# Optimization experiments

Measured on AMD Instinct MI355X. Metric: run time of the kernel, lower is better.

The kernel has to match this reference:

```python
import jax, jax.numpy as jnp
import numpy as np

N = 100000   # num_entities
R = 200      # num_relations
D = 128      # hidden_dim
B = 50       # num_bases = min(R, max(25, R//4))
E = 1600000  # num_edges (avg degree 16)
L = 2        # num_layers


def setup_inputs() -> dict:
    key = jax.random.key(0)
    ks = jax.random.split(key, 7)
    scale = 1.0 / np.sqrt(D)
    entity_emb = jax.random.normal(ks[0], (N, D), jnp.float32) * 0.05  # xavier-scale
    comp = jax.random.normal(ks[1], (L, R, B), jnp.float32) * (1.0 / np.sqrt(B))
    basis = jax.random.normal(ks[2], (L, B, D, D), jnp.float32) * scale
    root = jax.random.normal(ks[3], (L, D, D), jnp.float32) * scale
    bias = jnp.zeros((L, D), jnp.float32)
    edge_index = jax.random.randint(ks[4], (2, E), 0, N, dtype=jnp.int64)
    edge_type = jax.random.randint(ks[5], (E,), 0, R, dtype=jnp.int64)
    return dict(entity_emb=entity_emb, comp=comp, basis=basis, root=root,
                bias=bias, edge_index=edge_index, edge_type=edge_type)


def _rgcn_layer(x, comp_l, basis_l, root_l, bias_l, src, dst, etype):
    # Basis-decomposed relation-specific message: msg_e = x[src_e] @ (sum_b comp[etype_e, b] * basis[b])
    c = comp_l[etype]            # [E, B] per-edge basis coefficients
    x_src = x[src]               # [E, D] gathered source features

    def body(acc, inp):
        b_mat, c_b = inp         # b_mat: [D, D], c_b: [E]
        return acc + c_b[:, None] * (x_src @ b_mat), None

    msg0 = jnp.zeros((src.shape[0], x.shape[1]), x.dtype)
    msg, _ = jax.lax.scan(body, msg0, (basis_l, c.T))  # scan over B bases

    # PyG RGCNConv uses mean aggregation PER RELATION: normalize each edge by
    # the number of incoming edges of the same relation at its destination.
    key = dst * R + etype
    cnt = jnp.zeros(N * R, x.dtype).at[key].add(1.0)
    norm = 1.0 / jnp.maximum(cnt[key], 1.0)             # [E]
    agg = jax.ops.segment_sum(msg * norm[:, None], dst, num_segments=N)
    return agg + x @ root_l + bias_l


def reference(entity_emb, comp, basis, root, bias, edge_index, edge_type):
    src, dst = edge_index[0], edge_index[1]
    x = entity_emb
    for l in range(L):
        x = _rgcn_layer(x, comp[l], basis[l], root[l], bias[l], src, dst, edge_type)
        x = jax.nn.relu(x)
        # dropout(p=0.2) is identity in eval mode
    return x
```

## Files before the change

kernel.cpp:

```cpp
#include <hip/hip_runtime.h>
#include <hip/hip_bf16.h>
#include <stdint.h>

#define D_ 128
#define R_ 200
#define B_ 50
#define N_ 100000
#define TE 64
#define RG_ 4
#define MAXC 8

typedef __attribute__((ext_vector_type(8))) short s8b;
typedef __attribute__((ext_vector_type(4))) float f32x4;
typedef __attribute__((ext_vector_type(4))) uint u32x4;


__device__ __forceinline__ ushort f2bf(float f) {
  uint u = __float_as_uint(f);
  return (ushort)((u + 0x7fffu + ((u >> 16) & 1u)) >> 16);
}
__device__ __forceinline__ float bf2f(ushort u) {
  return __uint_as_float(((uint)u) << 16);
}


__global__ __launch_bounds__(256) void k_hist(const int* __restrict__ et, int E, int* __restrict__ hist) {
  __shared__ int h[R_];
  for (int i = threadIdx.x; i < R_; i += 256) h[i] = 0;
  __syncthreads();
  int base = blockIdx.x * 4096;
  for (int j = 0; j < 16; j++) {
    int i = base + j * 256 + threadIdx.x;
    if (i < E) atomicAdd(&h[et[i]], 1);
  }
  __syncthreads();
  for (int i = threadIdx.x; i < R_; i += 256) { int v = h[i]; if (v) atomicAdd(&hist[i], v); }
}

__global__ __launch_bounds__(256) void k_scanRel(const int* __restrict__ hist,
                                                 int* __restrict__ padOff, int* __restrict__ cursor) {
  __shared__ int s[256];
  int tid = threadIdx.x;
  int v = (tid < R_) ? ((hist[tid] + TE - 1) / TE) * TE : 0;
  s[tid] = v;
  __syncthreads();
  for (int off = 1; off < 256; off <<= 1) {
    int t = (tid >= off) ? s[tid - off] : 0;
    __syncthreads();
    s[tid] += t;
    __syncthreads();
  }
  if (tid < R_) { int e = s[tid] - v; padOff[tid] = e; cursor[tid] = e; }
  if (tid == R_ - 1) padOff[R_] = s[tid];
}

__global__ __launch_bounds__(256) void k_scatter(const int* __restrict__ src, const int* __restrict__ dst,
                                                 const int* __restrict__ et, int E,
                                                 int* __restrict__ cursor,
                                                 int2* __restrict__ srcdst, int* __restrict__ deg) {
  __shared__ int h[R_];
  __shared__ int gb[R_];
  for (int i = threadIdx.x; i < R_; i += 256) h[i] = 0;
  __syncthreads();
  int base = blockIdx.x * 4096;
  int lrank[16];
#pragma unroll
  for (int j = 0; j < 16; j++) {
    int i = base + j * 256 + threadIdx.x;
    lrank[j] = (i < E) ? atomicAdd(&h[et[i]], 1) : 0;
  }
  __syncthreads();
  for (int i = threadIdx.x; i < R_; i += 256) { int v = h[i]; gb[i] = v ? atomicAdd(&cursor[i], v) : 0; }
  __syncthreads();
#pragma unroll
  for (int j = 0; j < 16; j++) {
    int i = base + j * 256 + threadIdx.x;
    if (i < E) {
      int r = et[i], d = dst[i];
      int pos = gb[r] + lrank[j];
      int2 sd; sd.x = src[i]; sd.y = d;
      srcdst[pos] = sd;
      atomicAdd(&deg[d], 1);
    }
  }
}

__global__ __launch_bounds__(256) void k_tileRel(const int* __restrict__ padOff, int* __restrict__ tileRel, int uT) {
  int t = blockIdx.x * 256 + threadIdx.x;
  if (t >= uT) return;
  int base = t * TE;
  if (base >= padOff[R_]) { tileRel[t] = 0; return; }
  int lo = 0, hi = R_ - 1;
  while (lo < hi) { int mid = (lo + hi + 1) >> 1; if (padOff[mid] <= base) lo = mid; else hi = mid - 1; }
  tileRel[t] = lo;
}


__global__ __launch_bounds__(256) void k_degPart(const int* __restrict__ deg, int* __restrict__ blkSum) {
  __shared__ int ws_[4];
  int i = blockIdx.x * 256 + threadIdx.x;
  int v = (i < N_) ? deg[i] : 0;
#pragma unroll
  for (int off = 32; off >= 1; off >>= 1) v += __shfl_down(v, off);
  if ((threadIdx.x & 63) == 0) ws_[threadIdx.x >> 6] = v;
  __syncthreads();
  if (threadIdx.x == 0) blkSum[blockIdx.x] = ws_[0] + ws_[1] + ws_[2] + ws_[3];
}

__global__ __launch_bounds__(512) void k_scanBlk(const int* __restrict__ blkSum, int* __restrict__ blkOff, int nblk) {
  __shared__ int s[512];
  int tid = threadIdx.x;
  int v = (tid < nblk) ? blkSum[tid] : 0;
  s[tid] = v;
  __syncthreads();
  for (int off = 1; off < 512; off <<= 1) {
    int t = (tid >= off) ? s[tid - off] : 0;
    __syncthreads();
    s[tid] += t;
    __syncthreads();
  }
  if (tid < nblk) blkOff[tid] = s[tid] - v;
}

__global__ __launch_bounds__(256) void k_writeOff(const int* __restrict__ deg, const int* __restrict__ blkOff,
                                                  int* __restrict__ dstOff, int* __restrict__ cur) {
  __shared__ int s[256];
  int i = blockIdx.x * 256 + threadIdx.x;
  int tid = threadIdx.x;
  int v = (i < N_) ? deg[i] : 0;
  s[tid] = v;
  __syncthreads();
  for (int off = 1; off < 256; off <<= 1) {
    int t = (tid >= off) ? s[tid - off] : 0;
    __syncthreads();
    s[tid] += t;
    __syncthreads();
  }
  int e = blkOff[blockIdx.x] + s[tid] - v;
  if (i < N_) { dstOff[i] = e; cur[i] = e; }
  else if (i == N_) dstOff[N_] = e;
}

__global__ __launch_bounds__(256) void k_scatterDst(const int2* __restrict__ srcdst,
                                                    const int* __restrict__ padOff, int* __restrict__ cur,
                                                    int* __restrict__ posbuf, int plo, int phi) {
  int p = plo + blockIdx.x * 256 + threadIdx.x;
  if (p >= phi || p >= padOff[R_]) return;
  int d = srcdst[p].y;
  if (d < 0) return;
  int j = atomicAdd(&cur[d], 1);
  posbuf[j] = p;
}

__global__ __launch_bounds__(256) void k_copyBound(const int* __restrict__ cur, int* __restrict__ bnd) {
  int d = blockIdx.x * 256 + threadIdx.x;
  if (d < N_) bnd[d] = cur[d];
}


__global__ __launch_bounds__(256) void k_norm(const int* __restrict__ posbuf, const int* __restrict__ dstOff,
                                              const int* __restrict__ tileRel, float* __restrict__ normS) {
  __shared__ int rels[4][128];
  int d = blockIdx.x * 4 + (threadIdx.x >> 6);
  int sub = threadIdx.x >> 6;
  int l = threadIdx.x & 63;
  int s0 = 0, deg = 0;
  if (d < N_) { s0 = dstOff[d]; deg = dstOff[d + 1] - s0; }
  int cap = deg < 128 ? deg : 128;
  int myp[4]; int myr[4];
  for (int j = l, t = 0; j < cap; j += 64, ++t) {
    int p = posbuf[s0 + j];
    int r = tileRel[p >> 6];
    rels[sub][j] = r;
    if (t < 4) { myp[t] = p; myr[t] = r; }
  }
  __syncthreads();
  if (d >= N_) return;
  for (int j = l, t = 0; j < deg; j += 64, ++t) {
    int p, r;
    if (j < 128 && t < 4) { p = myp[t]; r = myr[t]; }
    else { p = posbuf[s0 + j]; r = tileRel[p >> 6]; }
    int cnt = 0;
    for (int k = 0; k < deg; k++) {
      int rk = (k < 128) ? rels[sub][k] : tileRel[posbuf[s0 + k] >> 6];
      cnt += (rk == r) ? 1 : 0;
    }
    normS[p] = 1.0f / (float)(cnt > 0 ? cnt : 1);
  }
}


__global__ __launch_bounds__(256) void k_computeW(const float* __restrict__ comp, const float* __restrict__ basis,
                                                  float* __restrict__ W) {
  __shared__ float c[B_];
  int r = blockIdx.x >> 6;
  int chunk = blockIdx.x & 63;
  if (threadIdx.x < B_) c[threadIdx.x] = comp[r * B_ + threadIdx.x];
  __syncthreads();
  int ij = chunk * 256 + threadIdx.x;
  float acc = 0.f;
#pragma unroll 10
  for (int b = 0; b < B_; b++) acc += c[b] * basis[b * (D_ * D_) + ij];
  W[r * (D_ * D_) + ij] = acc;
}

__global__ __launch_bounds__(256) void k_packW(const float* __restrict__ W, ushort* __restrict__ Wpack) {
  int r = blockIdx.x;
  const float* Wr = W + (size_t)r * (D_ * D_);
  ushort* out = Wpack + (size_t)r * (D_ * D_);
  for (int i = threadIdx.x; i < D_ * D_; i += 256) {
    int j = i & 7, l = (i >> 3) & 63, cg = (i >> 9) & 7, ks = i >> 12;
    int k = ks * 32 + (l >> 4) * 8 + j;
    int n = cg * 16 + (l & 15);
    out[i] = f2bf(Wr[k * D_ + n]);
  }
}

__global__ __launch_bounds__(256) void k_cast(const float* __restrict__ x, ushort* __restrict__ xb, int n8) {
  int i = blockIdx.x * 256 + threadIdx.x;
  if (i >= n8) return;
  const float4* xp = (const float4*)(x + (size_t)i * 8);
  float4 a = xp[0], b = xp[1];
  uint4 pk;
  pk.x = (uint)f2bf(a.x) | ((uint)f2bf(a.y) << 16);
  pk.y = (uint)f2bf(a.z) | ((uint)f2bf(a.w) << 16);
  pk.z = (uint)f2bf(b.x) | ((uint)f2bf(b.y) << 16);
  pk.w = (uint)f2bf(b.z) | ((uint)f2bf(b.w) << 16);
  *(uint4*)(xb + (size_t)i * 8) = pk;
}


__global__ __launch_bounds__(256, 2) void k_root_mfma(
    const ushort* __restrict__ xb, const ushort* __restrict__ rootPack,
    const float* __restrict__ bias, float* __restrict__ y, int nt) {
  __shared__ ushort Wl[D_ * D_];
  __shared__ float stg[4][16 * 132];
  int tstart = blockIdx.x * RG_;
  if (tstart >= nt) return;
  int tend = tstart + RG_; if (tend > nt) tend = nt;
  int w = threadIdx.x >> 6, l = threadIdx.x & 63;
  int q = l >> 4, tx = l & 15;
  int half = l >> 5, l32 = l & 31;
  float* st = stg[w];
  {
    const uint4* wp = (const uint4*)rootPack;
    uint4* wl = (uint4*)Wl;
#pragma unroll
    for (int i = 0; i < 8; ++i) wl[i * 256 + threadIdx.x] = wp[i * 256 + threadIdx.x];
  }
  float bv[8];
#pragma unroll
  for (int cg = 0; cg < 8; ++cg) bv[cg] = bias[cg * 16 + tx];
  s8b a0, a1, a2, a3;
  {
    int gr = tstart * TE + 16 * w + tx; if (gr >= N_) gr = N_ - 1;
    const s8b* xr = (const s8b*)(xb + (size_t)gr * D_);
    a0 = xr[q]; a1 = xr[4 + q]; a2 = xr[8 + q]; a3 = xr[12 + q];
  }
  __syncthreads();
  for (int tile = tstart; tile < tend; ++tile) {
    int base = tile * TE;
    s8b n0, n1, n2, n3;
    bool pre = (tile + 1 < tend);
    if (pre) {
      int gr = base + TE + 16 * w + tx; if (gr >= N_) gr = N_ - 1;
      const s8b* xn = (const s8b*)(xb + (size_t)gr * D_);
      n0 = xn[q]; n1 = xn[4 + q]; n2 = xn[8 + q]; n3 = xn[12 + q];
    }
    f32x4 acc[8];
#pragma unroll
    for (int cg = 0; cg < 8; ++cg) acc[cg] = (f32x4){0.f, 0.f, 0.f, 0.f};
#pragma unroll
    for (int cg = 0; cg < 8; ++cg) {
      s8b b0 = *(const s8b*)&Wl[((0 * 8 + cg) * 64 + l) * 8];
      s8b b1 = *(const s8b*)&Wl[((1 * 8 + cg) * 64 + l) * 8];
      s8b b2 = *(const s8b*)&Wl[((2 * 8 + cg) * 64 + l) * 8];
      s8b b3 = *(const s8b*)&Wl[((3 * 8 + cg) * 64 + l) * 8];
      acc[cg] = __builtin_amdgcn_mfma_f32_16x16x32_bf16(a0, b0, acc[cg], 0, 0, 0);
      acc[cg] = __builtin_amdgcn_mfma_f32_16x16x32_bf16(a1, b1, acc[cg], 0, 0, 0);
      acc[cg] = __builtin_amdgcn_mfma_f32_16x16x32_bf16(a2, b2, acc[cg], 0, 0, 0);
      acc[cg] = __builtin_amdgcn_mfma_f32_16x16x32_bf16(a3, b3, acc[cg], 0, 0, 0);
    }
#pragma unroll
    for (int cg = 0; cg < 8; ++cg)
#pragma unroll
      for (int r = 0; r < 4; ++r)
        st[(4 * q + r) * 132 + cg * 16 + tx] = acc[cg][r] + bv[cg];
    int grBase = base + 16 * w;
#pragma unroll
    for (int k = 0; k < 8; ++k) {
      int row = 2 * k + half;
      int gr = grBase + row;
      f32x4 v = *(const f32x4*)&st[row * 132 + l32 * 4];
      if (gr < N_) *(f32x4*)(y + (size_t)gr * D_ + l32 * 4) = v;
    }
    if (pre) { a0 = n0; a1 = n1; a2 = n2; a3 = n3; }
  }
}


__global__ __launch_bounds__(256, 4) void k_edges_mfma(
    const ushort* __restrict__ xb, const ushort* __restrict__ Wpack,
    const int2* __restrict__ srcdst, const float* __restrict__ normS,
    const int* __restrict__ tileRel, const int* __restrict__ padOff,
    ushort* __restrict__ msg, int tile0, int tile1, int G) {
  __shared__ ushort Wl[D_ * D_];
  __shared__ ushort stg[4][16 * 136];
  int padTot = padOff[R_];
  int w = threadIdx.x >> 6, l = threadIdx.x & 63;
  int q = l >> 4, tx = l & 15;
  int g = l >> 3, m = l & 7;
  ushort* st = stg[w];
  int curRel = -1;
  for (int tb = tile0 + blockIdx.x * G; tb < tile1; tb += gridDim.x * G) {
    if (tb * TE >= padTot) break;
    int tend = tb + G; if (tend > tile1) tend = tile1;
    s8b a0, a1, a2, a3;
    {
      int2 sd = srcdst[tb * TE + 16 * w + tx];
      int sr = sd.x < 0 ? 0 : sd.x;
      const s8b* xr = (const s8b*)(xb + (size_t)sr * D_);
      a0 = xr[q]; a1 = xr[4 + q]; a2 = xr[8 + q]; a3 = xr[12 + q];
    }
    for (int tile = tb; tile < tend; ++tile) {
      int base = tile * TE;
      if (base >= padTot) break;
      int rel = tileRel[tile];
      if (rel != curRel) {
        curRel = rel;
        __syncthreads();
        const uint4* wp = (const uint4*)(Wpack + (size_t)rel * (D_ * D_));
        uint4* wl = (uint4*)Wl;
#pragma unroll
        for (int i = 0; i < 8; ++i) wl[i * 256 + threadIdx.x] = wp[i * 256 + threadIdx.x];
        __syncthreads();
      }
      float nv[4];
#pragma unroll
      for (int r = 0; r < 4; ++r) nv[r] = normS[base + 16 * w + 4 * q + r];
      s8b n0, n1, n2, n3;
      int nb = base + TE;
      bool pre = (tile + 1 < tend) && (nb < padTot);
      if (pre) {
        int2 sd = srcdst[nb + 16 * w + tx];
        int sr = sd.x < 0 ? 0 : sd.x;
        const s8b* xn = (const s8b*)(xb + (size_t)sr * D_);
        n0 = xn[q]; n1 = xn[4 + q]; n2 = xn[8 + q]; n3 = xn[12 + q];
      }
      f32x4 acc[8];
#pragma unroll
      for (int cg = 0; cg < 8; ++cg) acc[cg] = (f32x4){0.f, 0.f, 0.f, 0.f};
#pragma unroll
      for (int cg = 0; cg < 8; ++cg) {
        s8b b0 = *(const s8b*)&Wl[((0 * 8 + cg) * 64 + l) * 8];
        s8b b1 = *(const s8b*)&Wl[((1 * 8 + cg) * 64 + l) * 8];
        s8b b2 = *(const s8b*)&Wl[((2 * 8 + cg) * 64 + l) * 8];
        s8b b3 = *(const s8b*)&Wl[((3 * 8 + cg) * 64 + l) * 8];
        acc[cg] = __builtin_amdgcn_mfma_f32_16x16x32_bf16(a0, b0, acc[cg], 0, 0, 0);
        acc[cg] = __builtin_amdgcn_mfma_f32_16x16x32_bf16(a1, b1, acc[cg], 0, 0, 0);
        acc[cg] = __builtin_amdgcn_mfma_f32_16x16x32_bf16(a2, b2, acc[cg], 0, 0, 0);
        acc[cg] = __builtin_amdgcn_mfma_f32_16x16x32_bf16(a3, b3, acc[cg], 0, 0, 0);
      }
#pragma unroll
      for (int cg = 0; cg < 8; ++cg)
#pragma unroll
        for (int r = 0; r < 4; ++r)
          st[(4 * q + r) * 136 + cg * 16 + tx] = f2bf(acc[cg][r] * nv[r]);
      ushort* mbase = msg + (size_t)(base - tile0 * TE + 16 * w) * D_;
#pragma unroll
      for (int jj = 0; jj < 2; ++jj)
#pragma unroll
        for (int hh = 0; hh < 2; ++hh) {
          int row = 8 * jj + g;
          u32x4 v = *(const u32x4*)&st[row * 136 + hh * 64 + m * 8];
          *(u32x4*)(mbase + (size_t)row * D_ + hh * 64 + m * 8) = v;
        }
      if (pre) { a0 = n0; a1 = n1; a2 = n2; a3 = n3; }
    }
  }
}


__global__ __launch_bounds__(256) void k_agg2(const ushort* __restrict__ msg, const int* __restrict__ posbuf,
                                              const int* __restrict__ jlo, const int* __restrict__ jhi,
                                              float* __restrict__ y, ushort* __restrict__ xbOut,
                                              int plo, int mode) {
  int d = blockIdx.x * 4 + (threadIdx.x >> 6);
  if (d >= N_) return;
  int l = threadIdx.x & 63, sub = l >> 4, tx = l & 15;
  int s0 = jlo[d], s1 = jhi[d];
  float acc[8];
#pragma unroll
  for (int i = 0; i < 8; ++i) acc[i] = 0.f;
  for (int j = s0 + sub; j < s1; j += 4) {
    int p = posbuf[j];
    u32x4 mv = *(const u32x4*)(msg + (((size_t)(p - plo)) << 7) + (tx << 3));
    acc[0] += bf2f((ushort)mv[0]); acc[1] += bf2f((ushort)(mv[0] >> 16));
    acc[2] += bf2f((ushort)mv[1]); acc[3] += bf2f((ushort)(mv[1] >> 16));
    acc[4] += bf2f((ushort)mv[2]); acc[5] += bf2f((ushort)(mv[2] >> 16));
    acc[6] += bf2f((ushort)mv[3]); acc[7] += bf2f((ushort)(mv[3] >> 16));
  }
#pragma unroll
  for (int i = 0; i < 8; ++i) {
    acc[i] += __shfl_xor(acc[i], 16);
    acc[i] += __shfl_xor(acc[i], 32);
  }
  if (sub == 0) {
    float* yp = y + (((size_t)d) << 7) + (tx << 3);
    float4 y0 = *(float4*)yp, y1 = *(float4*)(yp + 4);
    y0.x += acc[0]; y0.y += acc[1]; y0.z += acc[2]; y0.w += acc[3];
    y1.x += acc[4]; y1.y += acc[5]; y1.z += acc[6]; y1.w += acc[7];
    if (mode == 0) {
      *(float4*)yp = y0; *(float4*)(yp + 4) = y1;
    } else {
      y0.x = fmaxf(y0.x, 0.f); y0.y = fmaxf(y0.y, 0.f); y0.z = fmaxf(y0.z, 0.f); y0.w = fmaxf(y0.w, 0.f);
      y1.x = fmaxf(y1.x, 0.f); y1.y = fmaxf(y1.y, 0.f); y1.z = fmaxf(y1.z, 0.f); y1.w = fmaxf(y1.w, 0.f);
      if (mode == 1) {
        *(float4*)yp = y0; *(float4*)(yp + 4) = y1;
      } else {
        uint4 pk;
        pk.x = (uint)f2bf(y0.x) | ((uint)f2bf(y0.y) << 16);
        pk.y = (uint)f2bf(y0.z) | ((uint)f2bf(y0.w) << 16);
        pk.z = (uint)f2bf(y1.x) | ((uint)f2bf(y1.y) << 16);
        pk.w = (uint)f2bf(y1.z) | ((uint)f2bf(y1.w) << 16);
        *(uint4*)(xbOut + (((size_t)d) << 7) + (tx << 3)) = pk;
      }
    }
  }
}


extern "C" void kernel_launch(void* const* d_in, const int* in_sizes, int n_in,
                              void* d_out, int out_size, void* d_ws, size_t ws_size,
                              hipStream_t stream) {
  const float* entity = (const float*)d_in[0];
  const float* comp   = (const float*)d_in[1];
  const float* basis  = (const float*)d_in[2];
  const float* root   = (const float*)d_in[3];
  const float* bias   = (const float*)d_in[4];
  const int*   eidx   = (const int*)d_in[5];
  const int*   etype  = (const int*)d_in[6];
  const int E = in_sizes[6];
  const int* src = eidx;
  const int* dst = eidx + E;

  char* ws = (char*)d_ws;
  const size_t Epad = (size_t)E + (size_t)R_ * TE;
  const int uTiles = (E + TE - 1) / TE + R_;
  const int NBLK = (N_ + 1 + 255) / 256;
  auto al = [](size_t x) { return (x + 255) & ~(size_t)255; };

  size_t o_Wpack  = 0;
  size_t o_srcdst = al(o_Wpack + (size_t)(R_ + 1) * D_ * D_ * 2);
  size_t o_normS  = al(o_srcdst + Epad * 8);
  size_t o_posbuf = al(o_normS + Epad * 4);
  size_t o_degDst = al(o_posbuf + (size_t)E * 4);
  size_t o_dstOff = al(o_degDst + (size_t)N_ * 4);
  size_t o_cursD  = al(o_dstOff + (size_t)(N_ + 8) * 4);
  size_t o_bounds = al(o_cursD + (size_t)N_ * 4);
  size_t o_tileRel= al(o_bounds + (size_t)MAXC * N_ * 4);
  size_t o_small  = al(o_tileRel + (size_t)uTiles * 4);
  size_t o_y1     = al(o_small + 8192);
  size_t o_xb     = al(o_y1 + (size_t)N_ * D_ * 4);
  size_t o_msg    = al(o_xb + (size_t)N_ * D_ * 2);

  size_t o_Wf     = o_msg;

  ushort* Wpack  = (ushort*)(ws + o_Wpack);
  int2*   srcdst = (int2*)(ws + o_srcdst);
  float*  normS  = (float*)(ws + o_normS);
  int*    posbuf = (int*)(ws + o_posbuf);
  int*    degDst = (int*)(ws + o_degDst);
  int*    dstOff = (int*)(ws + o_dstOff);
  int*    cursD  = (int*)(ws + o_cursD);
  int*    bounds = (int*)(ws + o_bounds);
  int*    tileRel= (int*)(ws + o_tileRel);
  int*    hist   = (int*)(ws + o_small);
  int*    padOff = hist + 256;
  int*    cursor = hist + 512;
  int*    blkSum = hist + 768;
  int*    blkOff = hist + 1280;
  float*  y1     = (float*)(ws + o_y1);
  ushort* xb     = (ushort*)(ws + o_xb);
  float*  Wf     = (float*)(ws + o_Wf);
  ushort* msg    = (ushort*)(ws + o_msg);
  ushort* rootPack = Wpack + (size_t)R_ * D_ * D_;

  (void)hipMemsetAsync(ws + o_srcdst, 0xFF, Epad * 8, stream);
  (void)hipMemsetAsync(ws + o_degDst, 0, (size_t)N_ * 4, stream);
  (void)hipMemsetAsync(ws + o_small, 0, 8192, stream);

  int gH = (E + 4095) / 4096;
  k_hist<<<gH, 256, 0, stream>>>(etype, E, hist);
  k_scanRel<<<1, 256, 0, stream>>>(hist, padOff, cursor);
  k_scatter<<<gH, 256, 0, stream>>>(src, dst, etype, E, cursor, srcdst, degDst);
  k_tileRel<<<(uTiles + 255) / 256, 256, 0, stream>>>(padOff, tileRel, uTiles);
  k_degPart<<<NBLK, 256, 0, stream>>>(degDst, blkSum);
  k_scanBlk<<<1, 512, 0, stream>>>(blkSum, blkOff, NBLK);
  k_writeOff<<<NBLK, 256, 0, stream>>>(degDst, blkOff, dstOff, cursD);

  size_t cap = (ws_size > o_msg + 16384) ? (ws_size - o_msg) : (size_t)16384;
  size_t tileBytes = (size_t)TE * D_ * 2;
  long long maxT = (long long)(cap / tileBytes);
  if (maxT < 1) maxT = 1;
  int nch = (int)((uTiles + maxT - 1) / maxT);
  if (nch < 1) nch = 1;
  size_t totalMsg = (size_t)uTiles * tileBytes;
  int nchT = (int)((totalMsg + ((size_t)136 << 20) - 1) / ((size_t)136 << 20));
  if (nch < nchT) nch = nchT;
  if (nch > MAXC) nch = MAXC;
  int chunkTiles = (uTiles + nch - 1) / nch;
  nch = (uTiles + chunkTiles - 1) / chunkTiles;

  for (int c = 0; c < nch; c++) {
    int plo = c * chunkTiles * TE;
    int phi = (c + 1) * chunkTiles * TE; if (phi > uTiles * TE) phi = uTiles * TE;
    int gS = (phi - plo + 255) / 256;
    if (gS > 0)
      k_scatterDst<<<gS, 256, 0, stream>>>(srcdst, padOff, cursD, posbuf, plo, phi);
    k_copyBound<<<(N_ + 255) / 256, 256, 0, stream>>>(cursD, bounds + (size_t)c * N_);
  }

  k_norm<<<(N_ + 3) / 4, 256, 0, stream>>>(posbuf, dstOff, tileRel, normS);

  int ntR = (N_ + TE - 1) / TE;
  int gAgg = (N_ + 3) / 4;
  k_cast<<<(N_ * D_ / 8 + 255) / 256, 256, 0, stream>>>(entity, xb, N_ * D_ / 8);
  for (int l = 0; l < 2; l++) {
    float* yout = l ? (float*)d_out : y1;
    k_computeW<<<R_ * 64, 256, 0, stream>>>(comp + l * R_ * B_, basis + (size_t)l * B_ * D_ * D_, Wf);
    k_packW<<<R_, 256, 0, stream>>>(Wf, Wpack);
    k_packW<<<1, 256, 0, stream>>>(root + (size_t)l * D_ * D_, rootPack);
    k_root_mfma<<<(ntR + RG_ - 1) / RG_, 256, 0, stream>>>(xb, rootPack, bias + l * D_, yout, ntR);
    for (int c = 0; c < nch; c++) {
      int t0 = c * chunkTiles;
      int t1 = t0 + chunkTiles; if (t1 > uTiles) t1 = uTiles;
      int tiles = t1 - t0;
      int G = (tiles + 1023) / 1024; if (G < 4) G = 4;
      int gB = (tiles + G - 1) / G;
      k_edges_mfma<<<gB, 256, 0, stream>>>(xb, Wpack, srcdst, normS, tileRel, padOff, msg, t0, t1, G);
      const int* jlo = (c == 0) ? dstOff : bounds + (size_t)(c - 1) * N_;
      const int* jhi = bounds + (size_t)c * N_;
      int mode = (c == nch - 1) ? (l ? 1 : 2) : 0;
      k_agg2<<<gAgg, 256, 0, stream>>>(msg, posbuf, jlo, jhi, yout, xb, t0 * TE, mode);
    }
  }
}
```

Before: 1.040 ms.

## Build dst-sorted position buffer via per-chunk counts and ranks instead of atomic cursors

The per-destination counting moves into the relation scatter kernel. It now counts edges per chunk and destination and records each edge's rank within its chunk/destination bucket. Chunk base offsets per destination are derived from these counts, and posbuf is filled in a single atomic-free pass. This replaces the per-chunk scatterDst/copyBound launch loop, which did atomic cursor increments. The cost is an extra rank array, an MAXC*N count array and its memset, plus two small extra kernels.

```diff
diff --git a/kernel.cpp b/kernel.cpp
--- a/kernel.cpp
+++ b/kernel.cpp
@@ -57,7 +57,8 @@
 __global__ __launch_bounds__(256) void k_scatter(const int* __restrict__ src, const int* __restrict__ dst,
                                                  const int* __restrict__ et, int E,
                                                  int* __restrict__ cursor,
-                                                 int2* __restrict__ srcdst, int* __restrict__ deg) {
+                                                 int2* __restrict__ srcdst, int* __restrict__ rankS,
+                                                 int* __restrict__ cntCD, int chunkP) {
   __shared__ int h[R_];
   __shared__ int gb[R_];
   for (int i = threadIdx.x; i < R_; i += 256) h[i] = 0;
@@ -80,7 +81,8 @@
       int pos = gb[r] + lrank[j];
       int2 sd; sd.x = src[i]; sd.y = d;
       srcdst[pos] = sd;
-      atomicAdd(&deg[d], 1);
+      int c = pos / chunkP;
+      rankS[pos] = atomicAdd(&cntCD[c * N_ + d], 1);
     }
   }
 }
@@ -96,6 +98,14 @@
 }
 
 
+__global__ __launch_bounds__(256) void k_deg(const int* __restrict__ cntCD, int* __restrict__ deg, int nch) {
+  int d = blockIdx.x * 256 + threadIdx.x;
+  if (d >= N_) return;
+  int s = 0;
+  for (int c = 0; c < nch; ++c) s += cntCD[c * N_ + d];
+  deg[d] = s;
+}
+
 __global__ __launch_bounds__(256) void k_degPart(const int* __restrict__ deg, int* __restrict__ blkSum) {
   __shared__ int ws_[4];
   int i = blockIdx.x * 256 + threadIdx.x;
@@ -123,7 +133,7 @@
 }
 
 __global__ __launch_bounds__(256) void k_writeOff(const int* __restrict__ deg, const int* __restrict__ blkOff,
-                                                  int* __restrict__ dstOff, int* __restrict__ cur) {
+                                                  int* __restrict__ dstOff) {
   __shared__ int s[256];
   int i = blockIdx.x * 256 + threadIdx.x;
   int tid = threadIdx.x;
@@ -137,24 +147,27 @@
     __syncthreads();
   }
   int e = blkOff[blockIdx.x] + s[tid] - v;
-  if (i < N_) { dstOff[i] = e; cur[i] = e; }
+  if (i < N_) dstOff[i] = e;
   else if (i == N_) dstOff[N_] = e;
 }
 
-__global__ __launch_bounds__(256) void k_scatterDst(const int2* __restrict__ srcdst,
-                                                    const int* __restrict__ padOff, int* __restrict__ cur,
-                                                    int* __restrict__ posbuf, int plo, int phi) {
-  int p = plo + blockIdx.x * 256 + threadIdx.x;
-  if (p >= phi || p >= padOff[R_]) return;
+__global__ __launch_bounds__(256) void k_base(const int* __restrict__ cntCD, const int* __restrict__ dstOff,
+                                              int* __restrict__ base, int nch) {
+  int d = blockIdx.x * 256 + threadIdx.x;
+  if (d >= N_) return;
+  int b = dstOff[d];
+  for (int c = 0; c < nch; ++c) { base[c * N_ + d] = b; b += cntCD[c * N_ + d]; }
+}
+
+__global__ __launch_bounds__(256) void k_buildPos(const int2* __restrict__ srcdst, const int* __restrict__ rankS,
+                                                  const int* __restrict__ base, int* __restrict__ posbuf,
+                                                  int chunkP, int pTot) {
+  int p = blockIdx.x * 256 + threadIdx.x;
+  if (p >= pTot) return;
   int d = srcdst[p].y;
   if (d < 0) return;
-  int j = atomicAdd(&cur[d], 1);
-  posbuf[j] = p;
-}
-
-__global__ __launch_bounds__(256) void k_copyBound(const int* __restrict__ cur, int* __restrict__ bnd) {
-  int d = blockIdx.x * 256 + threadIdx.x;
-  if (d < N_) bnd[d] = cur[d];
+  int c = p / chunkP;
+  posbuf[base[c * N_ + d] + rankS[p]] = p;
 }
 
 
@@ -454,11 +467,12 @@
   size_t o_srcdst = al(o_Wpack + (size_t)(R_ + 1) * D_ * D_ * 2);
   size_t o_normS  = al(o_srcdst + Epad * 8);
   size_t o_posbuf = al(o_normS + Epad * 4);
-  size_t o_degDst = al(o_posbuf + (size_t)E * 4);
+  size_t o_rankS  = al(o_posbuf + (size_t)E * 4);
+  size_t o_degDst = al(o_rankS + Epad * 4);
   size_t o_dstOff = al(o_degDst + (size_t)N_ * 4);
-  size_t o_cursD  = al(o_dstOff + (size_t)(N_ + 8) * 4);
-  size_t o_bounds = al(o_cursD + (size_t)N_ * 4);
-  size_t o_tileRel= al(o_bounds + (size_t)MAXC * N_ * 4);
+  size_t o_base   = al(o_dstOff + (size_t)(N_ + 8) * 4);
+  size_t o_cntCD  = al(o_base + (size_t)MAXC * N_ * 4);
+  size_t o_tileRel= al(o_cntCD + (size_t)MAXC * N_ * 4);
   size_t o_small  = al(o_tileRel + (size_t)uTiles * 4);
   size_t o_y1     = al(o_small + 8192);
   size_t o_xb     = al(o_y1 + (size_t)N_ * D_ * 4);
@@ -470,10 +484,11 @@
   int2*   srcdst = (int2*)(ws + o_srcdst);
   float*  normS  = (float*)(ws + o_normS);
   int*    posbuf = (int*)(ws + o_posbuf);
+  int*    rankS  = (int*)(ws + o_rankS);
   int*    degDst = (int*)(ws + o_degDst);
   int*    dstOff = (int*)(ws + o_dstOff);
-  int*    cursD  = (int*)(ws + o_cursD);
-  int*    bounds = (int*)(ws + o_bounds);
+  int*    base_  = (int*)(ws + o_base);
+  int*    cntCD  = (int*)(ws + o_cntCD);
   int*    tileRel= (int*)(ws + o_tileRel);
   int*    hist   = (int*)(ws + o_small);
   int*    padOff = hist + 256;
@@ -485,19 +500,6 @@
   float*  Wf     = (float*)(ws + o_Wf);
   ushort* msg    = (ushort*)(ws + o_msg);
   ushort* rootPack = Wpack + (size_t)R_ * D_ * D_;
-
-  (void)hipMemsetAsync(ws + o_srcdst, 0xFF, Epad * 8, stream);
-  (void)hipMemsetAsync(ws + o_degDst, 0, (size_t)N_ * 4, stream);
-  (void)hipMemsetAsync(ws + o_small, 0, 8192, stream);
-
-  int gH = (E + 4095) / 4096;
-  k_hist<<<gH, 256, 0, stream>>>(etype, E, hist);
-  k_scanRel<<<1, 256, 0, stream>>>(hist, padOff, cursor);
-  k_scatter<<<gH, 256, 0, stream>>>(src, dst, etype, E, cursor, srcdst, degDst);
-  k_tileRel<<<(uTiles + 255) / 256, 256, 0, stream>>>(padOff, tileRel, uTiles);
-  k_degPart<<<NBLK, 256, 0, stream>>>(degDst, blkSum);
-  k_scanBlk<<<1, 512, 0, stream>>>(blkSum, blkOff, NBLK);
-  k_writeOff<<<NBLK, 256, 0, stream>>>(degDst, blkOff, dstOff, cursD);
 
   size_t cap = (ws_size > o_msg + 16384) ? (ws_size - o_msg) : (size_t)16384;
   size_t tileBytes = (size_t)TE * D_ * 2;
@@ -511,16 +513,23 @@
   if (nch > MAXC) nch = MAXC;
   int chunkTiles = (uTiles + nch - 1) / nch;
   nch = (uTiles + chunkTiles - 1) / chunkTiles;
-
-  for (int c = 0; c < nch; c++) {
-    int plo = c * chunkTiles * TE;
-    int phi = (c + 1) * chunkTiles * TE; if (phi > uTiles * TE) phi = uTiles * TE;
-    int gS = (phi - plo + 255) / 256;
-    if (gS > 0)
-      k_scatterDst<<<gS, 256, 0, stream>>>(srcdst, padOff, cursD, posbuf, plo, phi);
-    k_copyBound<<<(N_ + 255) / 256, 256, 0, stream>>>(cursD, bounds + (size_t)c * N_);
-  }
-
+  int chunkP = chunkTiles * TE;
+
+  (void)hipMemsetAsync(ws + o_srcdst, 0xFF, Epad * 8, stream);
+  (void)hipMemsetAsync(ws + o_cntCD, 0, (size_t)MAXC * N_ * 4, stream);
+  (void)hipMemsetAsync(ws + o_small, 0, 8192, stream);
+
+  int gH = (E + 4095) / 4096;
+  k_hist<<<gH, 256, 0, stream>>>(etype, E, hist);
+  k_scanRel<<<1, 256, 0, stream>>>(hist, padOff, cursor);
+  k_scatter<<<gH, 256, 0, stream>>>(src, dst, etype, E, cursor, srcdst, rankS, cntCD, chunkP);
+  k_tileRel<<<(uTiles + 255) / 256, 256, 0, stream>>>(padOff, tileRel, uTiles);
+  k_deg<<<(N_ + 255) / 256, 256, 0, stream>>>(cntCD, degDst, nch);
+  k_degPart<<<NBLK, 256, 0, stream>>>(degDst, blkSum);
+  k_scanBlk<<<1, 512, 0, stream>>>(blkSum, blkOff, NBLK);
+  k_writeOff<<<NBLK, 256, 0, stream>>>(degDst, blkOff, dstOff);
+  k_base<<<(N_ + 255) / 256, 256, 0, stream>>>(cntCD, dstOff, base_, nch);
+  k_buildPos<<<(uTiles * TE + 255) / 256, 256, 0, stream>>>(srcdst, rankS, base_, posbuf, chunkP, uTiles * TE);
   k_norm<<<(N_ + 3) / 4, 256, 0, stream>>>(posbuf, dstOff, tileRel, normS);
 
   int ntR = (N_ + TE - 1) / TE;
@@ -539,8 +548,8 @@
       int G = (tiles + 1023) / 1024; if (G < 4) G = 4;
       int gB = (tiles + G - 1) / G;
       k_edges_mfma<<<gB, 256, 0, stream>>>(xb, Wpack, srcdst, normS, tileRel, padOff, msg, t0, t1, G);
-      const int* jlo = (c == 0) ? dstOff : bounds + (size_t)(c - 1) * N_;
-      const int* jhi = bounds + (size_t)c * N_;
+      const int* jlo = base_ + (size_t)c * N_;
+      const int* jhi = (c == nch - 1) ? (dstOff + 1) : (base_ + (size_t)(c + 1) * N_);
       int mode = (c == nch - 1) ? (l ? 1 : 2) : 0;
       k_agg2<<<gAgg, 256, 0, stream>>>(msg, posbuf, jlo, jhi, yout, xb, t0 * TE, mode);
     }
```

Measured after the change: 973.7 us. -6.4%, faster.

## Partition edges by destination chunk so each chunk aggregates only its own nodes

Applied to the files above, without the earlier changes.

Edges are now bucketed by (destination chunk, relation) instead of by relation alone. Each message chunk therefore covers a disjoint range of destination nodes, and the aggregation kernel only visits that range instead of all nodes on every chunk, so the per-chunk bound arrays and read-modify-write passes go away. The dst-sorted position buffer is now built in one pass from per-edge ranks, replacing the chunked atomic scatter and bound copies. In exchange the edge records grow to int4, there are up to MAXC*R buckets and so more padding tiles, and a second bf16 activation buffer is added so the layer input is not overwritten while later chunks still read it.

```diff
diff --git a/kernel.cpp b/kernel.cpp
--- a/kernel.cpp
+++ b/kernel.cpp
@@ -9,6 +9,7 @@
 #define TE 64
 #define RG_ 4
 #define MAXC 8
+#define NBMAX (MAXC * R_)
 
 typedef __attribute__((ext_vector_type(8))) short s8b;
 typedef __attribute__((ext_vector_type(4))) float f32x4;
@@ -24,24 +25,126 @@
 }
 
 
-__global__ __launch_bounds__(256) void k_hist(const int* __restrict__ et, int E, int* __restrict__ hist) {
-  __shared__ int h[R_];
-  for (int i = threadIdx.x; i < R_; i += 256) h[i] = 0;
+__global__ __launch_bounds__(256) void k_hist(const int* __restrict__ dst, const int* __restrict__ et,
+                                              int E, int* __restrict__ hist, int DCH, int NB) {
+  __shared__ int h[NBMAX];
+  for (int i = threadIdx.x; i < NB; i += 256) h[i] = 0;
   __syncthreads();
   int base = blockIdx.x * 4096;
   for (int j = 0; j < 16; j++) {
     int i = base + j * 256 + threadIdx.x;
-    if (i < E) atomicAdd(&h[et[i]], 1);
-  }
-  __syncthreads();
-  for (int i = threadIdx.x; i < R_; i += 256) { int v = h[i]; if (v) atomicAdd(&hist[i], v); }
-}
-
-__global__ __launch_bounds__(256) void k_scanRel(const int* __restrict__ hist,
-                                                 int* __restrict__ padOff, int* __restrict__ cursor) {
+    if (i < E) {
+      int key = (dst[i] / DCH) * R_ + et[i];
+      atomicAdd(&h[key], 1);
+    }
+  }
+  __syncthreads();
+  for (int i = threadIdx.x; i < NB; i += 256) { int v = h[i]; if (v) atomicAdd(&hist[i], v); }
+}
+
+__global__ __launch_bounds__(1024) void k_scanRel(const int* __restrict__ hist,
+                                                  int* __restrict__ padOff, int* __restrict__ cursor, int NB) {
+  __shared__ int s[1024];
+  int tid = threadIdx.x;
+  int i0 = 2 * tid, i1 = 2 * tid + 1;
+  int v0 = (i0 < NB) ? ((hist[i0] + TE - 1) / TE) * TE : 0;
+  int v1 = (i1 < NB) ? ((hist[i1] + TE - 1) / TE) * TE : 0;
+  int v = v0 + v1;
+  s[tid] = v;
+  __syncthreads();
+  for (int off = 1; off < 1024; off <<= 1) {
+    int t = (tid >= off) ? s[tid - off] : 0;
+    __syncthreads();
+    s[tid] += t;
+    __syncthreads();
+  }
+  int e = s[tid] - v;
+  if (i0 < NB) { padOff[i0] = e; cursor[i0] = e; }
+  if (i1 < NB) { padOff[i1] = e + v0; cursor[i1] = e + v0; }
+  if (tid == 1023) padOff[NB] = s[1023];
+}
+
+__global__ __launch_bounds__(256) void k_scatter(const int* __restrict__ src, const int* __restrict__ dst,
+                                                 const int* __restrict__ et, int E,
+                                                 int* __restrict__ cursor,
+                                                 int4* __restrict__ sd4, int* __restrict__ cnt,
+                                                 int DCH, int NB) {
+  __shared__ int h[NBMAX];
+  __shared__ int gb[NBMAX];
+  for (int i = threadIdx.x; i < NB; i += 256) h[i] = 0;
+  __syncthreads();
+  int base = blockIdx.x * 4096;
+  int lrank[16];
+#pragma unroll
+  for (int j = 0; j < 16; j++) {
+    int i = base + j * 256 + threadIdx.x;
+    lrank[j] = 0;
+    if (i < E) {
+      int key = (dst[i] / DCH) * R_ + et[i];
+      lrank[j] = atomicAdd(&h[key], 1);
+    }
+  }
+  __syncthreads();
+  for (int i = threadIdx.x; i < NB; i += 256) { int v = h[i]; gb[i] = v ? atomicAdd(&cursor[i], v) : 0; }
+  __syncthreads();
+#pragma unroll
+  for (int j = 0; j < 16; j++) {
+    int i = base + j * 256 + threadIdx.x;
+    if (i < E) {
+      int d = dst[i];
+      int key = (d / DCH) * R_ + et[i];
+      int pos = gb[key] + lrank[j];
+      int rank = atomicAdd(&cnt[d], 1);
+      int4 sd; sd.x = src[i]; sd.y = d; sd.z = rank; sd.w = 0;
+      sd4[pos] = sd;
+    }
+  }
+}
+
+__global__ __launch_bounds__(256) void k_tileRel(const int* __restrict__ padOff, int* __restrict__ tileRel,
+                                                 int uT, int NB) {
+  int t = blockIdx.x * 256 + threadIdx.x;
+  if (t >= uT) return;
+  int base = t * TE;
+  if (base >= padOff[NB]) { tileRel[t] = 0; return; }
+  int lo = 0, hi = NB - 1;
+  while (lo < hi) { int mid = (lo + hi + 1) >> 1; if (padOff[mid] <= base) lo = mid; else hi = mid - 1; }
+  tileRel[t] = lo % R_;
+}
+
+
+__global__ __launch_bounds__(256) void k_degPart(const int* __restrict__ deg, int* __restrict__ blkSum) {
+  __shared__ int ws_[4];
+  int i = blockIdx.x * 256 + threadIdx.x;
+  int v = (i < N_) ? deg[i] : 0;
+#pragma unroll
+  for (int off = 32; off >= 1; off >>= 1) v += __shfl_down(v, off);
+  if ((threadIdx.x & 63) == 0) ws_[threadIdx.x >> 6] = v;
+  __syncthreads();
+  if (threadIdx.x == 0) blkSum[blockIdx.x] = ws_[0] + ws_[1] + ws_[2] + ws_[3];
+}
+
+__global__ __launch_bounds__(512) void k_scanBlk(const int* __restrict__ blkSum, int* __restrict__ blkOff, int nblk) {
+  __shared__ int s[512];
+  int tid = threadIdx.x;
+  int v = (tid < nblk) ? blkSum[tid] : 0;
+  s[tid] = v;
+  __syncthreads();
+  for (int off = 1; off < 512; off <<= 1) {
+    int t = (tid >= off) ? s[tid - off] : 0;
+    __syncthreads();
+    s[tid] += t;
+    __syncthreads();
+  }
+  if (tid < nblk) blkOff[tid] = s[tid] - v;
+}
+
+__global__ __launch_bounds__(256) void k_writeOff(const int* __restrict__ deg, const int* __restrict__ blkOff,
+                                                  int* __restrict__ dstOff) {
   __shared__ int s[256];
+  int i = blockIdx.x * 256 + threadIdx.x;
   int tid = threadIdx.x;
-  int v = (tid < R_) ? ((hist[tid] + TE - 1) / TE) * TE : 0;
+  int v = (i < N_) ? deg[i] : 0;
   s[tid] = v;
   __syncthreads();
   for (int off = 1; off < 256; off <<= 1) {
@@ -50,111 +153,18 @@
     s[tid] += t;
     __syncthreads();
   }
-  if (tid < R_) { int e = s[tid] - v; padOff[tid] = e; cursor[tid] = e; }
-  if (tid == R_ - 1) padOff[R_] = s[tid];
-}
-
-__global__ __launch_bounds__(256) void k_scatter(const int* __restrict__ src, const int* __restrict__ dst,
-                                                 const int* __restrict__ et, int E,
-                                                 int* __restrict__ cursor,
-                                                 int2* __restrict__ srcdst, int* __restrict__ deg) {
-  __shared__ int h[R_];
-  __shared__ int gb[R_];
-  for (int i = threadIdx.x; i < R_; i += 256) h[i] = 0;
-  __syncthreads();
-  int base = blockIdx.x * 4096;
-  int lrank[16];
-#pragma unroll
-  for (int j = 0; j < 16; j++) {
-    int i = base + j * 256 + threadIdx.x;
-    lrank[j] = (i < E) ? atomicAdd(&h[et[i]], 1) : 0;
-  }
-  __syncthreads();
-  for (int i = threadIdx.x; i < R_; i += 256) { int v = h[i]; gb[i] = v ? atomicAdd(&cursor[i], v) : 0; }
-  __syncthreads();
-#pragma unroll
-  for (int j = 0; j < 16; j++) {
-    int i = base + j * 256 + threadIdx.x;
-    if (i < E) {
-      int r = et[i], d = dst[i];
-      int pos = gb[r] + lrank[j];
-      int2 sd; sd.x = src[i]; sd.y = d;
-      srcdst[pos] = sd;
-      atomicAdd(&deg[d], 1);
-    }
-  }
-}
-
-__global__ __launch_bounds__(256) void k_tileRel(const int* __restrict__ padOff, int* __restrict__ tileRel, int uT) {
-  int t = blockIdx.x * 256 + threadIdx.x;
-  if (t >= uT) return;
-  int base = t * TE;
-  if (base >= padOff[R_]) { tileRel[t] = 0; return; }
-  int lo = 0, hi = R_ - 1;
-  while (lo < hi) { int mid = (lo + hi + 1) >> 1; if (padOff[mid] <= base) lo = mid; else hi = mid - 1; }
-  tileRel[t] = lo;
-}
-
-
-__global__ __launch_bounds__(256) void k_degPart(const int* __restrict__ deg, int* __restrict__ blkSum) {
-  __shared__ int ws_[4];
-  int i = blockIdx.x * 256 + threadIdx.x;
-  int v = (i < N_) ? deg[i] : 0;
-#pragma unroll
-  for (int off = 32; off >= 1; off >>= 1) v += __shfl_down(v, off);
-  if ((threadIdx.x & 63) == 0) ws_[threadIdx.x >> 6] = v;
-  __syncthreads();
-  if (threadIdx.x == 0) blkSum[blockIdx.x] = ws_[0] + ws_[1] + ws_[2] + ws_[3];
-}
-
-__global__ __launch_bounds__(512) void k_scanBlk(const int* __restrict__ blkSum, int* __restrict__ blkOff, int nblk) {
-  __shared__ int s[512];
-  int tid = threadIdx.x;
-  int v = (tid < nblk) ? blkSum[tid] : 0;
-  s[tid] = v;
-  __syncthreads();
-  for (int off = 1; off < 512; off <<= 1) {
-    int t = (tid >= off) ? s[tid - off] : 0;
-    __syncthreads();
-    s[tid] += t;
-    __syncthreads();
-  }
-  if (tid < nblk) blkOff[tid] = s[tid] - v;
-}
-
-__global__ __launch_bounds__(256) void k_writeOff(const int* __restrict__ deg, const int* __restrict__ blkOff,
-                                                  int* __restrict__ dstOff, int* __restrict__ cur) {
-  __shared__ int s[256];
-  int i = blockIdx.x * 256 + threadIdx.x;
-  int tid = threadIdx.x;
-  int v = (i < N_) ? deg[i] : 0;
-  s[tid] = v;
-  __syncthreads();
-  for (int off = 1; off < 256; off <<= 1) {
-    int t = (tid >= off) ? s[tid - off] : 0;
-    __syncthreads();
-    s[tid] += t;
-    __syncthreads();
-  }
   int e = blkOff[blockIdx.x] + s[tid] - v;
-  if (i < N_) { dstOff[i] = e; cur[i] = e; }
+  if (i < N_) dstOff[i] = e;
   else if (i == N_) dstOff[N_] = e;
 }
 
-__global__ __launch_bounds__(256) void k_scatterDst(const int2* __restrict__ srcdst,
-                                                    const int* __restrict__ padOff, int* __restrict__ cur,
-                                                    int* __restrict__ posbuf, int plo, int phi) {
-  int p = plo + blockIdx.x * 256 + threadIdx.x;
-  if (p >= phi || p >= padOff[R_]) return;
-  int d = srcdst[p].y;
-  if (d < 0) return;
-  int j = atomicAdd(&cur[d], 1);
-  posbuf[j] = p;
-}
-
-__global__ __launch_bounds__(256) void k_copyBound(const int* __restrict__ cur, int* __restrict__ bnd) {
-  int d = blockIdx.x * 256 + threadIdx.x;
-  if (d < N_) bnd[d] = cur[d];
+__global__ __launch_bounds__(256) void k_buildPos(const int4* __restrict__ sd4, const int* __restrict__ dstOff,
+                                                  int* __restrict__ posbuf, int pTot) {
+  int p = blockIdx.x * 256 + threadIdx.x;
+  if (p >= pTot) return;
+  int4 sd = sd4[p];
+  if (sd.y < 0) return;
+  posbuf[dstOff[sd.y] + sd.z] = p;
 }
 
 
@@ -301,30 +311,32 @@
 
 __global__ __launch_bounds__(256, 4) void k_edges_mfma(
     const ushort* __restrict__ xb, const ushort* __restrict__ Wpack,
-    const int2* __restrict__ srcdst, const float* __restrict__ normS,
+    const int4* __restrict__ sd4, const float* __restrict__ normS,
     const int* __restrict__ tileRel, const int* __restrict__ padOff,
-    ushort* __restrict__ msg, int tile0, int tile1, int G) {
+    ushort* __restrict__ msg, int c) {
   __shared__ ushort Wl[D_ * D_];
   __shared__ ushort stg[4][16 * 136];
-  int padTot = padOff[R_];
+  int b0 = padOff[c * R_], b1 = padOff[(c + 1) * R_];
+  int tile0 = b0 >> 6, tile1 = b1 >> 6;
+  int tiles = tile1 - tile0;
+  if (tiles <= 0) return;
+  int G = (tiles + (int)gridDim.x - 1) / (int)gridDim.x;
   int w = threadIdx.x >> 6, l = threadIdx.x & 63;
   int q = l >> 4, tx = l & 15;
   int g = l >> 3, m = l & 7;
   ushort* st = stg[w];
   int curRel = -1;
-  for (int tb = tile0 + blockIdx.x * G; tb < tile1; tb += gridDim.x * G) {
-    if (tb * TE >= padTot) break;
+  for (int tb = tile0 + blockIdx.x * G; tb < tile1; tb += (int)gridDim.x * G) {
     int tend = tb + G; if (tend > tile1) tend = tile1;
     s8b a0, a1, a2, a3;
     {
-      int2 sd = srcdst[tb * TE + 16 * w + tx];
+      int4 sd = sd4[tb * TE + 16 * w + tx];
       int sr = sd.x < 0 ? 0 : sd.x;
       const s8b* xr = (const s8b*)(xb + (size_t)sr * D_);
       a0 = xr[q]; a1 = xr[4 + q]; a2 = xr[8 + q]; a3 = xr[12 + q];
     }
     for (int tile = tb; tile < tend; ++tile) {
       int base = tile * TE;
-      if (base >= padTot) break;
       int rel = tileRel[tile];
       if (rel != curRel) {
         curRel = rel;
@@ -339,10 +351,9 @@
 #pragma unroll
       for (int r = 0; r < 4; ++r) nv[r] = normS[base + 16 * w + 4 * q + r];
       s8b n0, n1, n2, n3;
-      int nb = base + TE;
-      bool pre = (tile + 1 < tend) && (nb < padTot);
+      bool pre = (tile + 1 < tend);
       if (pre) {
-        int2 sd = srcdst[nb + 16 * w + tx];
+        int4 sd = sd4[base + TE + 16 * w + tx];
         int sr = sd.x < 0 ? 0 : sd.x;
         const s8b* xn = (const s8b*)(xb + (size_t)sr * D_);
         n0 = xn[q]; n1 = xn[4 + q]; n2 = xn[8 + q]; n3 = xn[12 + q];
@@ -352,21 +363,21 @@
       for (int cg = 0; cg < 8; ++cg) acc[cg] = (f32x4){0.f, 0.f, 0.f, 0.f};
 #pragma unroll
       for (int cg = 0; cg < 8; ++cg) {
-        s8b b0 = *(const s8b*)&Wl[((0 * 8 + cg) * 64 + l) * 8];
-        s8b b1 = *(const s8b*)&Wl[((1 * 8 + cg) * 64 + l) * 8];
-        s8b b2 = *(const s8b*)&Wl[((2 * 8 + cg) * 64 + l) * 8];
-        s8b b3 = *(const s8b*)&Wl[((3 * 8 + cg) * 64 + l) * 8];
-        acc[cg] = __builtin_amdgcn_mfma_f32_16x16x32_bf16(a0, b0, acc[cg], 0, 0, 0);
-        acc[cg] = __builtin_amdgcn_mfma_f32_16x16x32_bf16(a1, b1, acc[cg], 0, 0, 0);
-        acc[cg] = __builtin_amdgcn_mfma_f32_16x16x32_bf16(a2, b2, acc[cg], 0, 0, 0);
-        acc[cg] = __builtin_amdgcn_mfma_f32_16x16x32_bf16(a3, b3, acc[cg], 0, 0, 0);
+        s8b b0v = *(const s8b*)&Wl[((0 * 8 + cg) * 64 + l) * 8];
+        s8b b1v = *(const s8b*)&Wl[((1 * 8 + cg) * 64 + l) * 8];
+        s8b b2v = *(const s8b*)&Wl[((2 * 8 + cg) * 64 + l) * 8];
+        s8b b3v = *(const s8b*)&Wl[((3 * 8 + cg) * 64 + l) * 8];
+        acc[cg] = __builtin_amdgcn_mfma_f32_16x16x32_bf16(a0, b0v, acc[cg], 0, 0, 0);
+        acc[cg] = __builtin_amdgcn_mfma_f32_16x16x32_bf16(a1, b1v, acc[cg], 0, 0, 0);
+        acc[cg] = __builtin_amdgcn_mfma_f32_16x16x32_bf16(a2, b2v, acc[cg], 0, 0, 0);
+        acc[cg] = __builtin_amdgcn_mfma_f32_16x16x32_bf16(a3, b3v, acc[cg], 0, 0, 0);
       }
 #pragma unroll
       for (int cg = 0; cg < 8; ++cg)
 #pragma unroll
         for (int r = 0; r < 4; ++r)
           st[(4 * q + r) * 136 + cg * 16 + tx] = f2bf(acc[cg][r] * nv[r]);
-      ushort* mbase = msg + (size_t)(base - tile0 * TE + 16 * w) * D_;
+      ushort* mbase = msg + (size_t)(base - b0 + 16 * w) * D_;
 #pragma unroll
       for (int jj = 0; jj < 2; ++jj)
 #pragma unroll
@@ -382,13 +393,14 @@
 
 
 __global__ __launch_bounds__(256) void k_agg2(const ushort* __restrict__ msg, const int* __restrict__ posbuf,
-                                              const int* __restrict__ jlo, const int* __restrict__ jhi,
+                                              const int* __restrict__ dstOff, const int* __restrict__ padOff,
                                               float* __restrict__ y, ushort* __restrict__ xbOut,
-                                              int plo, int mode) {
-  int d = blockIdx.x * 4 + (threadIdx.x >> 6);
-  if (d >= N_) return;
+                                              int c, int dlo, int dhi, int mode) {
+  int d = dlo + blockIdx.x * 4 + (threadIdx.x >> 6);
+  if (d >= dhi) return;
+  int plo = padOff[c * R_];
   int l = threadIdx.x & 63, sub = l >> 4, tx = l & 15;
-  int s0 = jlo[d], s1 = jhi[d];
+  int s0 = dstOff[d], s1 = dstOff[d + 1];
   float acc[8];
 #pragma unroll
   for (int i = 0; i < 8; ++i) acc[i] = 0.f;
@@ -408,23 +420,19 @@
   if (sub == 0) {
     float* yp = y + (((size_t)d) << 7) + (tx << 3);
     float4 y0 = *(float4*)yp, y1 = *(float4*)(yp + 4);
-    y0.x += acc[0]; y0.y += acc[1]; y0.z += acc[2]; y0.w += acc[3];
-    y1.x += acc[4]; y1.y += acc[5]; y1.z += acc[6]; y1.w += acc[7];
-    if (mode == 0) {
+    y0.x = fmaxf(y0.x + acc[0], 0.f); y0.y = fmaxf(y0.y + acc[1], 0.f);
+    y0.z = fmaxf(y0.z + acc[2], 0.f); y0.w = fmaxf(y0.w + acc[3], 0.f);
+    y1.x = fmaxf(y1.x + acc[4], 0.f); y1.y = fmaxf(y1.y + acc[5], 0.f);
+    y1.z = fmaxf(y1.z + acc[6], 0.f); y1.w = fmaxf(y1.w + acc[7], 0.f);
+    if (mode == 1) {
       *(float4*)yp = y0; *(float4*)(yp + 4) = y1;
     } else {
-      y0.x = fmaxf(y0.x, 0.f); y0.y = fmaxf(y0.y, 0.f); y0.z = fmaxf(y0.z, 0.f); y0.w = fmaxf(y0.w, 0.f);
-      y1.x = fmaxf(y1.x, 0.f); y1.y = fmaxf(y1.y, 0.f); y1.z = fmaxf(y1.z, 0.f); y1.w = fmaxf(y1.w, 0.f);
-      if (mode == 1) {
-        *(float4*)yp = y0; *(float4*)(yp + 4) = y1;
-      } else {
-        uint4 pk;
-        pk.x = (uint)f2bf(y0.x) | ((uint)f2bf(y0.y) << 16);
-        pk.y = (uint)f2bf(y0.z) | ((uint)f2bf(y0.w) << 16);
-        pk.z = (uint)f2bf(y1.x) | ((uint)f2bf(y1.y) << 16);
-        pk.w = (uint)f2bf(y1.z) | ((uint)f2bf(y1.w) << 16);
-        *(uint4*)(xbOut + (((size_t)d) << 7) + (tx << 3)) = pk;
-      }
+      uint4 pk;
+      pk.x = (uint)f2bf(y0.x) | ((uint)f2bf(y0.y) << 16);
+      pk.y = (uint)f2bf(y0.z) | ((uint)f2bf(y0.w) << 16);
+      pk.z = (uint)f2bf(y1.x) | ((uint)f2bf(y1.y) << 16);
+      pk.w = (uint)f2bf(y1.z) | ((uint)f2bf(y1.w) << 16);
+      *(uint4*)(xbOut + (((size_t)d) << 7) + (tx << 3)) = pk;
     }
   }
 }
@@ -445,104 +453,87 @@
   const int* dst = eidx + E;
 
   char* ws = (char*)d_ws;
-  const size_t Epad = (size_t)E + (size_t)R_ * TE;
-  const int uTiles = (E + TE - 1) / TE + R_;
+  const int baseTiles = (E + TE - 1) / TE;
+  const int uTmax = baseTiles + NBMAX;
   const int NBLK = (N_ + 1 + 255) / 256;
   auto al = [](size_t x) { return (x + 255) & ~(size_t)255; };
 
   size_t o_Wpack  = 0;
-  size_t o_srcdst = al(o_Wpack + (size_t)(R_ + 1) * D_ * D_ * 2);
-  size_t o_normS  = al(o_srcdst + Epad * 8);
-  size_t o_posbuf = al(o_normS + Epad * 4);
-  size_t o_degDst = al(o_posbuf + (size_t)E * 4);
-  size_t o_dstOff = al(o_degDst + (size_t)N_ * 4);
-  size_t o_cursD  = al(o_dstOff + (size_t)(N_ + 8) * 4);
-  size_t o_bounds = al(o_cursD + (size_t)N_ * 4);
-  size_t o_tileRel= al(o_bounds + (size_t)MAXC * N_ * 4);
-  size_t o_small  = al(o_tileRel + (size_t)uTiles * 4);
-  size_t o_y1     = al(o_small + 8192);
+  size_t o_sd4    = al(o_Wpack + (size_t)(R_ + 1) * D_ * D_ * 2);
+  size_t o_normS  = al(o_sd4 + (size_t)uTmax * TE * 16);
+  size_t o_posbuf = al(o_normS + (size_t)uTmax * TE * 4);
+  size_t o_cnt    = al(o_posbuf + (size_t)E * 4);
+  size_t o_dstOff = al(o_cnt + (size_t)N_ * 4);
+  size_t o_tileRel= al(o_dstOff + (size_t)(N_ + 8) * 4);
+  size_t o_small  = al(o_tileRel + (size_t)uTmax * 4);
+  size_t o_y1     = al(o_small + 32768);
   size_t o_xb     = al(o_y1 + (size_t)N_ * D_ * 4);
-  size_t o_msg    = al(o_xb + (size_t)N_ * D_ * 2);
-
+  size_t o_xb2    = al(o_xb + (size_t)N_ * D_ * 2);
+  size_t o_msg    = al(o_xb2 + (size_t)N_ * D_ * 2);
   size_t o_Wf     = o_msg;
 
   ushort* Wpack  = (ushort*)(ws + o_Wpack);
-  int2*   srcdst = (int2*)(ws + o_srcdst);
+  int4*   sd4    = (int4*)(ws + o_sd4);
   float*  normS  = (float*)(ws + o_normS);
   int*    posbuf = (int*)(ws + o_posbuf);
-  int*    degDst = (int*)(ws + o_degDst);
+  int*    cnt    = (int*)(ws + o_cnt);
   int*    dstOff = (int*)(ws + o_dstOff);
-  int*    cursD  = (int*)(ws + o_cursD);
-  int*    bounds = (int*)(ws + o_bounds);
   int*    tileRel= (int*)(ws + o_tileRel);
   int*    hist   = (int*)(ws + o_small);
-  int*    padOff = hist + 256;
-  int*    cursor = hist + 512;
-  int*    blkSum = hist + 768;
-  int*    blkOff = hist + 1280;
+  int*    padOff = hist + 1664;
+  int*    cursor = hist + 3328;
+  int*    blkSum = hist + 4992;
+  int*    blkOff = hist + 5504;
   float*  y1     = (float*)(ws + o_y1);
   ushort* xb     = (ushort*)(ws + o_xb);
+  ushort* xb2    = (ushort*)(ws + o_xb2);
   float*  Wf     = (float*)(ws + o_Wf);
   ushort* msg    = (ushort*)(ws + o_msg);
   ushort* rootPack = Wpack + (size_t)R_ * D_ * D_;
 
-  (void)hipMemsetAsync(ws + o_srcdst, 0xFF, Epad * 8, stream);
-  (void)hipMemsetAsync(ws + o_degDst, 0, (size_t)N_ * 4, stream);
-  (void)hipMemsetAsync(ws + o_small, 0, 8192, stream);
-
-  int gH = (E + 4095) / 4096;
-  k_hist<<<gH, 256, 0, stream>>>(etype, E, hist);
-  k_scanRel<<<1, 256, 0, stream>>>(hist, padOff, cursor);
-  k_scatter<<<gH, 256, 0, stream>>>(src, dst, etype, E, cursor, srcdst, degDst);
-  k_tileRel<<<(uTiles + 255) / 256, 256, 0, stream>>>(padOff, tileRel, uTiles);
-  k_degPart<<<NBLK, 256, 0, stream>>>(degDst, blkSum);
-  k_scanBlk<<<1, 512, 0, stream>>>(blkSum, blkOff, NBLK);
-  k_writeOff<<<NBLK, 256, 0, stream>>>(degDst, blkOff, dstOff, cursD);
-
   size_t cap = (ws_size > o_msg + 16384) ? (ws_size - o_msg) : (size_t)16384;
   size_t tileBytes = (size_t)TE * D_ * 2;
   long long maxT = (long long)(cap / tileBytes);
-  if (maxT < 1) maxT = 1;
-  int nch = (int)((uTiles + maxT - 1) / maxT);
-  if (nch < 1) nch = 1;
-  size_t totalMsg = (size_t)uTiles * tileBytes;
-  int nchT = (int)((totalMsg + ((size_t)136 << 20) - 1) / ((size_t)136 << 20));
-  if (nch < nchT) nch = nchT;
-  if (nch > MAXC) nch = MAXC;
-  int chunkTiles = (uTiles + nch - 1) / nch;
-  nch = (uTiles + chunkTiles - 1) / chunkTiles;
-
-  for (int c = 0; c < nch; c++) {
-    int plo = c * chunkTiles * TE;
-    int phi = (c + 1) * chunkTiles * TE; if (phi > uTiles * TE) phi = uTiles * TE;
-    int gS = (phi - plo + 255) / 256;
-    if (gS > 0)
-      k_scatterDst<<<gS, 256, 0, stream>>>(srcdst, padOff, cursD, posbuf, plo, phi);
-    k_copyBound<<<(N_ + 255) / 256, 256, 0, stream>>>(cursD, bounds + (size_t)c * N_);
-  }
-
+  int nch = MAXC;
+  for (int n = 1; n <= MAXC; ++n) {
+    long long expT = (long long)baseTiles / n + R_ + TE;
+    if (expT * 3 / 2 <= maxT && expT * (long long)tileBytes <= (136LL << 20)) { nch = n; break; }
+  }
+  const int NB = nch * R_;
+  const int uT = baseTiles + NB;
+  const int DCH = (N_ + nch - 1) / nch;
+  const size_t EpadU = (size_t)uT * TE;
+
+  (void)hipMemsetAsync(ws + o_sd4, 0xFF, EpadU * 16, stream);
+  (void)hipMemsetAsync(ws + o_cnt, 0, (size_t)N_ * 4, stream);
+  (void)hipMemsetAsync(ws + o_small, 0, 32768, stream);
+
+  int gH = (E + 4095) / 4096;
+  k_hist<<<gH, 256, 0, stream>>>(dst, etype, E, hist, DCH, NB);
+  k_scanRel<<<1, 1024, 0, stream>>>(hist, padOff, cursor, NB);
+  k_scatter<<<gH, 256, 0, stream>>>(src, dst, etype, E, cursor, sd4, cnt, DCH, NB);
+  k_tileRel<<<(uT + 255) / 256, 256, 0, stream>>>(padOff, tileRel, uT, NB);
+  k_degPart<<<NBLK, 256, 0, stream>>>(cnt, blkSum);
+  k_scanBlk<<<1, 512, 0, stream>>>(blkSum, blkOff, NBLK);
+  k_writeOff<<<NBLK, 256, 0, stream>>>(cnt, blkOff, dstOff);
+  k_buildPos<<<(int)((EpadU + 255) / 256), 256, 0, stream>>>(sd4, dstOff, posbuf, (int)EpadU);
   k_norm<<<(N_ + 3) / 4, 256, 0, stream>>>(posbuf, dstOff, tileRel, normS);
 
   int ntR = (N_ + TE - 1) / TE;
-  int gAgg = (N_ + 3) / 4;
+  int gAgg = (DCH + 3) / 4;
   k_cast<<<(N_ * D_ / 8 + 255) / 256, 256, 0, stream>>>(entity, xb, N_ * D_ / 8);
   for (int l = 0; l < 2; l++) {
+    const ushort* xin = l ? xb2 : xb;
     float* yout = l ? (float*)d_out : y1;
     k_computeW<<<R_ * 64, 256, 0, stream>>>(comp + l * R_ * B_, basis + (size_t)l * B_ * D_ * D_, Wf);
     k_packW<<<R_, 256, 0, stream>>>(Wf, Wpack);
     k_packW<<<1, 256, 0, stream>>>(root + (size_t)l * D_ * D_, rootPack);
-    k_root_mfma<<<(ntR + RG_ - 1) / RG_, 256, 0, stream>>>(xb, rootPack, bias + l * D_, yout, ntR);
+    k_root_mfma<<<(ntR + RG_ - 1) / RG_, 256, 0, stream>>>(xin, rootPack, bias + l * D_, yout, ntR);
     for (int c = 0; c < nch; c++) {
-      int t0 = c * chunkTiles;
-      int t1 = t0 + chunkTiles; if (t1 > uTiles) t1 = uTiles;
-      int tiles = t1 - t0;
-      int G = (tiles + 1023) / 1024; if (G < 4) G = 4;
-      int gB = (tiles + G - 1) / G;
-      k_edges_mfma<<<gB, 256, 0, stream>>>(xb, Wpack, srcdst, normS, tileRel, padOff, msg, t0, t1, G);
-      const int* jlo = (c == 0) ? dstOff : bounds + (size_t)(c - 1) * N_;
-      const int* jhi = bounds + (size_t)c * N_;
-      int mode = (c == nch - 1) ? (l ? 1 : 2) : 0;
-      k_agg2<<<gAgg, 256, 0, stream>>>(msg, posbuf, jlo, jhi, yout, xb, t0 * TE, mode);
-    }
-  }
-}
+      k_edges_mfma<<<1024, 256, 0, stream>>>(xin, Wpack, sd4, normS, tileRel, padOff, msg, c);
+      int dlo = c * DCH;
+      int dhi = (c + 1) * DCH; if (dhi > N_) dhi = N_;
+      k_agg2<<<gAgg, 256, 0, stream>>>(msg, posbuf, dstOff, padOff, yout, xb2, c, dlo, dhi, l ? 1 : 2);
+    }
+  }
+}
```

Measured after the change: 1.008 ms. 1.03x faster.
